# Kernel optimization log

Measured on AMD Instinct MI355X. Metric: run time of the kernel, lower is better.

Reference implementation:

```python
import jax, jax.numpy as jnp
import numpy as np

DIM = 2048
HEADS = 16
HD = DIM // HEADS  # 128
EPS = 1e-5


def layernorm(t, w, b):
    # FloatLayerNorm: LayerNorm computed in float32 over last dim
    t32 = t.astype(jnp.float32)
    mu = jnp.mean(t32, axis=-1, keepdims=True)
    var = jnp.mean(jnp.square(t32 - mu), axis=-1, keepdims=True)
    y = (t32 - mu) * jax.lax.rsqrt(var + EPS)
    return (y * w + b).astype(t.dtype)


def rope(t, f_real, f_imag):
    # t: [b, s, h, hd]; frequencies in cis form, sliced to seq length
    b, s, h, hd = t.shape
    tr = t.astype(jnp.float32).reshape(b, s, h, hd // 2, 2)
    xr, xi = tr[..., 0], tr[..., 1]
    fr = f_real[:s][None, :, None, :]  # [1, s, 1, hd/2]
    fi = f_imag[:s][None, :, None, :]
    o_r = xr * fr - xi * fi
    o_i = xr * fi + xi * fr
    return jnp.stack([o_r, o_i], axis=-1).reshape(b, s, h, hd).astype(t.dtype)


def proj_norm_rope(t, Wq, Wk, Wv, qn_w, qn_b, kn_w, kn_b, f_real, f_imag):
    b, s, _ = t.shape
    q = layernorm(t @ Wq, qn_w, qn_b).reshape(b, s, HEADS, HD)
    k = layernorm(t @ Wk, kn_w, kn_b).reshape(b, s, HEADS, HD)
    v = (t @ Wv).reshape(b, s, HEADS, HD)
    q = rope(q, f_real, f_imag)
    k = rope(k, f_real, f_imag)
    return q, k, v


def sdpa(q, k, v, scale):
    # q,k,v: [b, s, h, hd] -> out [b, s, h, hd]
    scores = jnp.einsum('bqhd,bkhd->bhqk', q, k) * scale
    probs = jax.nn.softmax(scores, axis=-1)
    return jnp.einsum('bhqk,bkhd->bqhd', probs, v)


def setup_inputs() -> dict:
    key = jax.random.key(0)
    ks = jax.random.split(key, 14)
    d = {
        'c': jax.random.normal(ks[0], (2, 256, DIM), jnp.float32),
        'x': jax.random.normal(ks[1], (2, 1792, DIM), jnp.float32),
        'f_real': jax.random.normal(ks[2], (2048, HD // 2), jnp.float32),
        'f_imag': jax.random.normal(ks[3], (2048, HD // 2), jnp.float32),
    }
    sc = 1.0 / np.sqrt(DIM)
    for i, name in enumerate(['Wq', 'Wk', 'Wv', 'Wo', 'W2q', 'W2k', 'W2v', 'W2o']):
        d[name] = jax.random.normal(ks[4 + i], (DIM, DIM), jnp.float32) * sc
    for name in ['qn_w', 'kn_w', 'q2n_w', 'k2n_w']:
        d[name] = jnp.ones((DIM,), jnp.float32)
    for name in ['qn_b', 'kn_b', 'q2n_b', 'k2n_b']:
        d[name] = jnp.zeros((DIM,), jnp.float32)
    return d


def reference(c, x, f_real, f_imag, Wq, Wk, Wv, Wo, W2q, W2k, W2v, W2o,
              qn_w, qn_b, kn_w, kn_b, q2n_w, q2n_b, k2n_w, k2n_b):
    s1 = c.shape[1]
    c_q, c_k, c_v = proj_norm_rope(c, Wq, Wk, Wv, qn_w, qn_b, kn_w, kn_b, f_real, f_imag)
    x_q, x_k, x_v = proj_norm_rope(x, W2q, W2k, W2v, q2n_w, q2n_b, k2n_w, k2n_b, f_real, f_imag)
    q = jnp.concatenate([c_q, x_q], axis=1)
    k = jnp.concatenate([c_k, x_k], axis=1)
    v = jnp.concatenate([c_v, x_v], axis=1)
    out = sdpa(q, k, v, scale=1.0 / np.sqrt(HD))  # scale_by_num_heads=True
    b, s, _, _ = out.shape
    out = out.reshape(b, s, DIM)
    c_out = out[:, :s1] @ Wo
    x_out = out[:, s1:] @ W2o
    return c_out, x_out
```

## Files before the change

kernel.cpp:

```cpp
#include <hip/hip_runtime.h>

typedef __attribute__((ext_vector_type(8))) short short8;
typedef __attribute__((ext_vector_type(4))) float f32x4;
typedef __attribute__((ext_vector_type(16))) float f32x16;

#define DEV __device__ __forceinline__

DEV unsigned short f2bf(float f) {
  unsigned int u; __builtin_memcpy(&u, &f, 4);
  u = (u + 0x7FFFu + ((u >> 16) & 1u)) >> 16;
  return (unsigned short)u;
}
DEV float bf2f(unsigned short h) {
  unsigned int u = ((unsigned int)h) << 16;
  float f; __builtin_memcpy(&f, &u, 4);
  return f;
}
DEV unsigned int cvtpk(float lo, float hi_) {
  unsigned int r;
  asm("v_cvt_pk_bf16_f32 %0, %1, %2" : "=v"(r) : "v"(lo), "v"(hi_));
  return r;
}

DEV void gload_lds16(const void* g, void* l) {
  __builtin_amdgcn_global_load_lds(
      (const __attribute__((address_space(1))) void*)g,
      (__attribute__((address_space(3))) void*)l, 16, 0, 0);
}

DEV f32x16 mfma32(short8 a, short8 b, f32x16 c) {
  return __builtin_amdgcn_mfma_f32_32x32x16_bf16(a, b, c, 0, 0, 0);
}

__global__ __launch_bounds__(256) void conv_tb(const float* __restrict__ c,
                                               const float* __restrict__ x,
                                               unsigned short* __restrict__ tb) {
  int row = blockIdx.x;
  int b = row >> 11, s = row & 2047;
  const float* src = (s < 256) ? (c + (size_t)(b * 256 + s) * 2048)
                               : (x + (size_t)(b * 1792 + (s - 256)) * 2048);
  int t = threadIdx.x;
  float4 v0 = *(const float4*)&src[t * 8];
  float4 v1 = *(const float4*)&src[t * 8 + 4];
  union { unsigned short us[8]; uint4 u; } pk;
  pk.us[0] = f2bf(v0.x); pk.us[1] = f2bf(v0.y); pk.us[2] = f2bf(v0.z); pk.us[3] = f2bf(v0.w);
  pk.us[4] = f2bf(v1.x); pk.us[5] = f2bf(v1.y); pk.us[6] = f2bf(v1.z); pk.us[7] = f2bf(v1.w);
  *(uint4*)&tb[(size_t)row * 2048 + t * 8] = pk.u;
}

__global__ __launch_bounds__(256) void trans_w(
    const float* __restrict__ w0, const float* __restrict__ w1,
    const float* __restrict__ w2, const float* __restrict__ w3,
    const float* __restrict__ w4, const float* __restrict__ w5,
    const float* __restrict__ w6, const float* __restrict__ w7,
    unsigned short* __restrict__ dstbase) {
  const float* W;
  switch (blockIdx.z) {
    case 0: W = w0; break; case 1: W = w1; break; case 2: W = w2; break; case 3: W = w3; break;
    case 4: W = w4; break; case 5: W = w5; break; case 6: W = w6; break; default: W = w7; break;
  }
  unsigned short* Wt = dstbase + (size_t)blockIdx.z * 2048 * 2048;
  __shared__ float tile[64][65];
  int n0 = blockIdx.x * 64, k0 = blockIdx.y * 64;
  int j = threadIdx.x & 63, i0 = threadIdx.x >> 6;
#pragma unroll
  for (int p = 0; p < 16; ++p) {
    int i = i0 + p * 4;
    tile[i][j] = W[(size_t)(k0 + i) * 2048 + n0 + j];
  }
  __syncthreads();
#pragma unroll
  for (int p = 0; p < 16; ++p) {
    int i = i0 + p * 4;
    Wt[(size_t)(n0 + i) * 2048 + k0 + j] = f2bf(tile[j][i]);
  }
}

__global__ __launch_bounds__(256) void gemm_qkv3(
    const unsigned short* __restrict__ A,
    const unsigned short* __restrict__ Wt,
    unsigned short* __restrict__ out) {
  __shared__ __align__(16) unsigned short As[128 * 32];
  __shared__ __align__(16) unsigned short Bs[128 * 32];
  const size_t M2 = 2048ull * 2048ull;
  const int which = blockIdx.x >> 4;
  const int m0 = blockIdx.y * 128, n0 = (blockIdx.x & 15) * 128;
  const unsigned short* Bt = Wt + (size_t)(((m0 & 2047) < 256) ? which : which + 4) * M2;
  unsigned short* C = out + (size_t)which * (4096ull * 2048ull);
  const int tid = threadIdx.x, wid = tid >> 6, lane = tid & 63;
  const int g = lane >> 4, l15 = lane & 15;
  const int wm = wid >> 1, wn = wid & 1;
  const int srow = lane >> 2, skk = (lane & 3) * 8;
  f32x4 acc[4][4] = {};
  for (int k0 = 0; k0 < 2048; k0 += 32) {
#pragma unroll
    for (int rep = 0; rep < 2; ++rep) {
      int ia = wid * 2 + rep;
      gload_lds16(&A[(size_t)(m0 + ia * 16 + srow) * 2048 + k0 + skk], (char*)As + ia * 1024);
      gload_lds16(&Bt[(size_t)(n0 + ia * 16 + srow) * 2048 + k0 + skk], (char*)Bs + ia * 1024);
    }
    __syncthreads();
    short8 a[4], bb[4];
#pragma unroll
    for (int mf = 0; mf < 4; ++mf) a[mf] = *(const short8*)&As[(wm * 64 + mf * 16 + l15) * 32 + g * 8];
#pragma unroll
    for (int nf = 0; nf < 4; ++nf) bb[nf] = *(const short8*)&Bs[(wn * 64 + nf * 16 + l15) * 32 + g * 8];
#pragma unroll
    for (int mf = 0; mf < 4; ++mf)
#pragma unroll
      for (int nf = 0; nf < 4; ++nf)
        acc[mf][nf] = __builtin_amdgcn_mfma_f32_16x16x32_bf16(a[mf], bb[nf], acc[mf][nf], 0, 0, 0);
    __syncthreads();
  }
#pragma unroll
  for (int mf = 0; mf < 4; ++mf)
#pragma unroll
    for (int r = 0; r < 4; ++r) {
      int row = m0 + wm * 64 + mf * 16 + 4 * g + r;
#pragma unroll
      for (int nf = 0; nf < 4; ++nf)
        C[(size_t)row * 2048 + n0 + wn * 64 + nf * 16 + l15] = f2bf(acc[mf][nf][r]);
    }
}

__global__ __launch_bounds__(256) void gemm_out(
    const unsigned short* __restrict__ A,
    const unsigned short* __restrict__ B1t,
    const unsigned short* __restrict__ B2t,
    float* __restrict__ Co) {
  __shared__ __align__(16) unsigned short As[128 * 32];
  __shared__ __align__(16) unsigned short Bs[128 * 32];
  const int m0 = blockIdx.y * 128, n0 = blockIdx.x * 128;
  const unsigned short* Bt = ((m0 & 2047) < 256) ? B1t : B2t;
  const int tid = threadIdx.x, wid = tid >> 6, lane = tid & 63;
  const int g = lane >> 4, l15 = lane & 15;
  const int wm = wid >> 1, wn = wid & 1;
  const int srow = lane >> 2, skk = (lane & 3) * 8;
  f32x4 acc[4][4] = {};
  for (int k0 = 0; k0 < 2048; k0 += 32) {
#pragma unroll
    for (int rep = 0; rep < 2; ++rep) {
      int ia = wid * 2 + rep;
      gload_lds16(&A[(size_t)(m0 + ia * 16 + srow) * 2048 + k0 + skk], (char*)As + ia * 1024);
      gload_lds16(&Bt[(size_t)(n0 + ia * 16 + srow) * 2048 + k0 + skk], (char*)Bs + ia * 1024);
    }
    __syncthreads();
    short8 a[4], bb[4];
#pragma unroll
    for (int mf = 0; mf < 4; ++mf) a[mf] = *(const short8*)&As[(wm * 64 + mf * 16 + l15) * 32 + g * 8];
#pragma unroll
    for (int nf = 0; nf < 4; ++nf) bb[nf] = *(const short8*)&Bs[(wn * 64 + nf * 16 + l15) * 32 + g * 8];
#pragma unroll
    for (int mf = 0; mf < 4; ++mf)
#pragma unroll
      for (int nf = 0; nf < 4; ++nf)
        acc[mf][nf] = __builtin_amdgcn_mfma_f32_16x16x32_bf16(a[mf], bb[nf], acc[mf][nf], 0, 0, 0);
    __syncthreads();
  }
#pragma unroll
  for (int mf = 0; mf < 4; ++mf)
#pragma unroll
    for (int r = 0; r < 4; ++r) {
      int row = m0 + wm * 64 + mf * 16 + 4 * g + r;
      int b = row >> 11, s = row & 2047;
      size_t dst = (s < 256) ? ((size_t)b * 256 + s) * 2048
                             : 1048576ull + ((size_t)b * 1792 + (s - 256)) * 2048;
#pragma unroll
      for (int nf = 0; nf < 4; ++nf)
        Co[dst + n0 + wn * 64 + nf * 16 + l15] = acc[mf][nf][r];
    }
}

__global__ __launch_bounds__(256) void ln_rope(
    const unsigned short* __restrict__ P,
    const float* __restrict__ w1, const float* __restrict__ b1,
    const float* __restrict__ w2, const float* __restrict__ b2,
    const float* __restrict__ fre, const float* __restrict__ fim,
    unsigned short* __restrict__ Oa, float oscale) {
  int row = blockIdx.x;
  int b = row >> 11, s = row & 2047;
  int pos = (s < 256) ? s : s - 256;
  const float* w = (s < 256) ? w1 : w2;
  const float* bb = (s < 256) ? b1 : b2;
  int t = threadIdx.x, lane = t & 63, wid = t >> 6;
  int col = t * 8;
  uint4 raw = *(const uint4*)&P[(size_t)row * 2048 + col];
  const unsigned short* rp = (const unsigned short*)&raw;
  float xv[8];
#pragma unroll
  for (int j = 0; j < 8; ++j) xv[j] = bf2f(rp[j]);
  float s1 = 0.f, s2 = 0.f;
#pragma unroll
  for (int j = 0; j < 8; ++j) { s1 += xv[j]; s2 += xv[j] * xv[j]; }
#pragma unroll
  for (int off = 32; off; off >>= 1) { s1 += __shfl_xor(s1, off); s2 += __shfl_xor(s2, off); }
  __shared__ float red1[4], red2[4];
  if (lane == 0) { red1[wid] = s1; red2[wid] = s2; }
  __syncthreads();
  s1 = red1[0] + red1[1] + red1[2] + red1[3];
  s2 = red2[0] + red2[1] + red2[2] + red2[3];
  float mean = s1 * (1.f / 2048.f);
  float var = s2 * (1.f / 2048.f) - mean * mean;
  float rs = rsqrtf(var + 1e-5f);
  float4 wv0 = *(const float4*)&w[col], wv1 = *(const float4*)&w[col + 4];
  float4 bv0 = *(const float4*)&bb[col], bv1 = *(const float4*)&bb[col + 4];
  float y[8];
  y[0] = (xv[0] - mean) * rs * wv0.x + bv0.x; y[1] = (xv[1] - mean) * rs * wv0.y + bv0.y;
  y[2] = (xv[2] - mean) * rs * wv0.z + bv0.z; y[3] = (xv[3] - mean) * rs * wv0.w + bv0.w;
  y[4] = (xv[4] - mean) * rs * wv1.x + bv1.x; y[5] = (xv[5] - mean) * rs * wv1.y + bv1.y;
  y[6] = (xv[6] - mean) * rs * wv1.z + bv1.z; y[7] = (xv[7] - mean) * rs * wv1.w + bv1.w;
#pragma unroll
  for (int j = 0; j < 8; ++j) y[j] *= oscale;
  int hd0 = col & 127;
  int i0 = hd0 >> 1;
  float4 fr = *(const float4*)&fre[(size_t)pos * 64 + i0];
  float4 fi = *(const float4*)&fim[(size_t)pos * 64 + i0];
  union { unsigned short us[8]; uint4 u; } pk;
  pk.us[0] = f2bf(y[0] * fr.x - y[1] * fi.x); pk.us[1] = f2bf(y[0] * fi.x + y[1] * fr.x);
  pk.us[2] = f2bf(y[2] * fr.y - y[3] * fi.y); pk.us[3] = f2bf(y[2] * fi.y + y[3] * fr.y);
  pk.us[4] = f2bf(y[4] * fr.z - y[5] * fi.z); pk.us[5] = f2bf(y[4] * fi.z + y[5] * fr.z);
  pk.us[6] = f2bf(y[6] * fr.w - y[7] * fi.w); pk.us[7] = f2bf(y[6] * fi.w + y[7] * fr.w);
  int h = col >> 7;
  *(uint4*)&Oa[((size_t)(b * 16 + h) * 2048 + s) * 128 + hd0] = pk.u;
}

__global__ __launch_bounds__(256) void v_trans(const unsigned short* __restrict__ vp,
                                               unsigned short* __restrict__ va) {
  int bh = blockIdx.y;
  int b = bh >> 4, h = bh & 15;
  int s0 = blockIdx.x * 64;
  __shared__ unsigned short tile[64][128];
  int tid = threadIdx.x;
#pragma unroll
  for (int p = 0; p < 4; ++p) {
    int s = p * 16 + (tid >> 4);
    int d0 = (tid & 15) * 8;
    *(uint4*)&tile[s][d0] = *(const uint4*)&vp[((size_t)b * 2048 + s0 + s) * 2048 + h * 128 + d0];
  }
  __syncthreads();
#pragma unroll
  for (int p = 0; p < 4; ++p) {
    int d = p * 32 + (tid >> 3);
    int soff = (tid & 7) * 8;
    union { unsigned short us[8]; uint4 u; } pk;
#pragma unroll
    for (int u = 0; u < 8; ++u) pk.us[u] = tile[soff + u][d];
    *(uint4*)&va[((size_t)(b * 16 + h) * 128 + d) * 2048 + s0 + soff] = pk.u;
  }
}

#define THR_LOG2 11.5f

__global__ __launch_bounds__(512) void attn_kernel(
    const unsigned short* __restrict__ Q,
    const unsigned short* __restrict__ Kb,
    const unsigned short* __restrict__ Vt,
    unsigned short* __restrict__ O) {
  __shared__ __align__(16) unsigned short smem[32768];
  const int q0 = blockIdx.x * 256;
  const int h = blockIdx.y, b = blockIdx.z;
  const int tid = threadIdx.x, wid = tid >> 6, lane = tid & 63;
  const int l31 = lane & 31, hi = lane >> 5;
  const size_t base = (size_t)(b * 16 + h) * 2048 * 128;
  const unsigned short* kbase = Kb + base;
  const unsigned short* vbase = Vt + base;

  const int qrow = q0 + wid * 32 + l31;
  short8 qf[8];
#pragma unroll
  for (int ks = 0; ks < 8; ++ks)
    qf[ks] = *(const short8*)&Q[base + (size_t)qrow * 128 + ks * 16 + hi * 8];

  f32x16 o_acc[4] = {};
  float m_run = -1e30f, l_run = 0.f;

#define STAGE(cur, kv0)                                                              \
  {                                                                                  \
_Pragma("unroll")                                                                    \
    for (int p = 0; p < 2; ++p) {                                                    \
      int slot = p * 512 + wid * 64 + lane;                                          \
      int row = slot >> 4;                                                           \
      int u = (slot & 15) ^ (row & 7);                                               \
      gload_lds16(&kbase[(size_t)((kv0) + row) * 128 + u * 8],                       \
                  (char*)(smem + (cur) * 16384) + (p * 512 + wid * 64) * 16);        \
    }                                                                                \
_Pragma("unroll")                                                                    \
    for (int p = 0; p < 2; ++p) {                                                    \
      int slot = p * 512 + wid * 64 + lane;                                          \
      int d = slot >> 3;                                                             \
      int u = (slot & 7) ^ (d & 7);                                                  \
      gload_lds16(&vbase[(size_t)d * 2048 + (kv0) + u * 8],                          \
                  (char*)(smem + (cur) * 16384 + 8192) + (p * 512 + wid * 64) * 16); \
    }                                                                                \
  }

  STAGE(0, 0)

#pragma unroll 1
  for (int t = 0; t < 32; ++t) {
    const int cur = t & 1;
    if (t < 31) {
      STAGE(cur ^ 1, (t + 1) * 64)
      asm volatile("s_waitcnt vmcnt(4)" ::: "memory");
    } else {
      asm volatile("s_waitcnt vmcnt(0)" ::: "memory");
    }
    __builtin_amdgcn_s_barrier();

    const char* Ksb = (const char*)(smem + cur * 16384);
    const char* Vsb = (const char*)(smem + cur * 16384 + 8192);

    f32x16 sT0 = {}, sT1 = {};
    __builtin_amdgcn_s_setprio(1);
#pragma unroll
    for (int ks = 0; ks < 8; ++ks) {
      int unit = ks * 2 + hi;
      int r0 = l31;
      short8 kf0 = *(const short8*)(Ksb + ((r0 * 16 + (unit ^ (r0 & 7))) << 4));
      sT0 = mfma32(kf0, qf[ks], sT0);
      int r1 = 32 + l31;
      short8 kf1 = *(const short8*)(Ksb + ((r1 * 16 + (unit ^ (r1 & 7))) << 4));
      sT1 = mfma32(kf1, qf[ks], sT1);
    }
    __builtin_amdgcn_s_setprio(0);

    float mx = sT0[0];
#pragma unroll
    for (int r = 1; r < 16; ++r) mx = fmaxf(mx, sT0[r]);
#pragma unroll
    for (int r = 0; r < 16; ++r) mx = fmaxf(mx, sT1[r]);
    mx = fmaxf(mx, __shfl_xor(mx, 32));
    if (!__all(mx <= m_run + THR_LOG2)) {
      float mn = fmaxf(m_run, mx);
      float corr = __builtin_exp2f(m_run - mn);
      m_run = mn;
      l_run *= corr;
#pragma unroll
      for (int di = 0; di < 4; ++di)
#pragma unroll
        for (int r = 0; r < 16; ++r) o_acc[di][r] *= corr;
    }
    float ts = 0.f;
#pragma unroll
    for (int r = 0; r < 16; ++r) { sT0[r] = __builtin_exp2f(sT0[r] - m_run); ts += sT0[r]; }
#pragma unroll
    for (int r = 0; r < 16; ++r) { sT1[r] = __builtin_exp2f(sT1[r] - m_run); ts += sT1[r]; }
    ts += __shfl_xor(ts, 32);
    l_run += ts;

    unsigned int w0[8], w1[8];
#pragma unroll
    for (int j = 0; j < 8; ++j) {
      w0[j] = cvtpk(sT0[2 * j], sT0[2 * j + 1]);
      w1[j] = cvtpk(sT1[2 * j], sT1[2 * j + 1]);
    }
    unsigned int y0[4], y1[4];
    y0[0] = __shfl_xor((int)(hi ? w0[0] : w0[2]), 32);
    y0[1] = __shfl_xor((int)(hi ? w0[1] : w0[3]), 32);
    y0[2] = __shfl_xor((int)(hi ? w0[4] : w0[6]), 32);
    y0[3] = __shfl_xor((int)(hi ? w0[5] : w0[7]), 32);
    y1[0] = __shfl_xor((int)(hi ? w1[0] : w1[2]), 32);
    y1[1] = __shfl_xor((int)(hi ? w1[1] : w1[3]), 32);
    y1[2] = __shfl_xor((int)(hi ? w1[4] : w1[6]), 32);
    y1[3] = __shfl_xor((int)(hi ? w1[5] : w1[7]), 32);
    union { unsigned int u[4]; short8 s8; } pf[2][2];
    pf[0][0].u[0] = hi ? y0[0] : w0[0]; pf[0][0].u[1] = hi ? y0[1] : w0[1];
    pf[0][0].u[2] = hi ? w0[2] : y0[0]; pf[0][0].u[3] = hi ? w0[3] : y0[1];
    pf[0][1].u[0] = hi ? y0[2] : w0[4]; pf[0][1].u[1] = hi ? y0[3] : w0[5];
    pf[0][1].u[2] = hi ? w0[6] : y0[2]; pf[0][1].u[3] = hi ? w0[7] : y0[3];
    pf[1][0].u[0] = hi ? y1[0] : w1[0]; pf[1][0].u[1] = hi ? y1[1] : w1[1];
    pf[1][0].u[2] = hi ? w1[2] : y1[0]; pf[1][0].u[3] = hi ? w1[3] : y1[1];
    pf[1][1].u[0] = hi ? y1[2] : w1[4]; pf[1][1].u[1] = hi ? y1[3] : w1[5];
    pf[1][1].u[2] = hi ? w1[6] : y1[2]; pf[1][1].u[3] = hi ? w1[7] : y1[3];

    __builtin_amdgcn_s_setprio(1);
#pragma unroll
    for (int di = 0; di < 4; ++di) {
      int row = di * 32 + l31;
      int sw = row & 7;
#pragma unroll
      for (int kb = 0; kb < 2; ++kb)
#pragma unroll
        for (int ks2 = 0; ks2 < 2; ++ks2) {
          int unit = kb * 4 + ks2 * 2 + hi;
          short8 vf = *(const short8*)(Vsb + ((row * 8 + (unit ^ sw)) << 4));
          o_acc[di] = mfma32(vf, pf[kb][ks2].s8, o_acc[di]);
        }
    }
    __builtin_amdgcn_s_setprio(0);
    __builtin_amdgcn_s_barrier();
  }

  float inv = 1.0f / l_run;
  char* ow = (char*)smem + wid * 8192;
#pragma unroll
  for (int di = 0; di < 4; ++di)
#pragma unroll
    for (int rg = 0; rg < 4; ++rg) {
      unsigned int lo = cvtpk(o_acc[di][rg * 4 + 0] * inv, o_acc[di][rg * 4 + 1] * inv);
      unsigned int hi_w = cvtpk(o_acc[di][rg * 4 + 2] * inv, o_acc[di][rg * 4 + 3] * inv);
      int byte = (l31 * 256 + di * 64 + rg * 16 + hi * 8) ^ ((l31 & 7) << 4);
      *(unsigned long long*)(ow + byte) =
          ((unsigned long long)hi_w << 32) | (unsigned long long)lo;
    }
  size_t obase = ((size_t)b * 2048 + q0 + wid * 32) * 2048 + (size_t)h * 128;
#pragma unroll
  for (int it = 0; it < 8; ++it) {
    int q = it * 4 + (lane >> 4);
    int d0 = (lane & 15) * 8;
    int byte = (q * 256 + d0 * 2) ^ ((q & 7) << 4);
    uint4 val = *(const uint4*)(ow + byte);
    *(uint4*)&O[obase + (size_t)q * 2048 + d0] = val;
  }
}

extern "C" void kernel_launch(void* const* d_in, const int* in_sizes, int n_in,
                              void* d_out, int out_size, void* d_ws, size_t ws_size,
                              hipStream_t stream) {
  (void)in_sizes; (void)n_in; (void)out_size; (void)ws_size;
  const float* c = (const float*)d_in[0];
  const float* x = (const float*)d_in[1];
  const float* fre = (const float*)d_in[2];
  const float* fim = (const float*)d_in[3];

  char* ws = (char*)d_ws;
  const size_t M2 = 2048ull * 2048ull;
  unsigned short* tb = (unsigned short*)ws;
  unsigned short* Wt = (unsigned short*)(ws + 16777216ull);
  unsigned short* qkv = (unsigned short*)(ws + 83886080ull);
  unsigned short* qp = qkv;
  unsigned short* kp = (unsigned short*)(ws + 100663296ull);
  unsigned short* vp = (unsigned short*)(ws + 117440512ull);
  unsigned short* qa = (unsigned short*)(ws + 134217728ull);
  unsigned short* ka = (unsigned short*)(ws + 150994944ull);
  unsigned short* va = (unsigned short*)(ws + 167772160ull);
  unsigned short* attn_out = qp;

  conv_tb<<<4096, 256, 0, stream>>>(c, x, tb);
  trans_w<<<dim3(32, 32, 8), 256, 0, stream>>>(
      (const float*)d_in[4], (const float*)d_in[5], (const float*)d_in[6], (const float*)d_in[7],
      (const float*)d_in[8], (const float*)d_in[9], (const float*)d_in[10], (const float*)d_in[11],
      Wt);
  gemm_qkv3<<<dim3(48, 32), 256, 0, stream>>>(tb, Wt, qkv);
  ln_rope<<<4096, 256, 0, stream>>>(qp, (const float*)d_in[12], (const float*)d_in[16],
                                    (const float*)d_in[14], (const float*)d_in[18], fre, fim, qa,
                                    0.08838834764831845f * 1.4426950408889634f);
  ln_rope<<<4096, 256, 0, stream>>>(kp, (const float*)d_in[13], (const float*)d_in[17],
                                    (const float*)d_in[15], (const float*)d_in[19], fre, fim, ka,
                                    1.0f);
  v_trans<<<dim3(32, 32), 256, 0, stream>>>(vp, va);
  attn_kernel<<<dim3(8, 16, 2), 512, 0, stream>>>(qa, ka, va, attn_out);
  gemm_out<<<dim3(16, 32), 256, 0, stream>>>(attn_out, Wt + 3 * M2, Wt + 7 * M2, (float*)d_out);
}
```

Measured before the change: 351.9 us.

## Rewrite QKV GEMM as 256x256-tile, 8-wave, double-buffered pipelined kernel

Replaces the 128x128, 4-wave QKV projection GEMM with a 256x256-tile, 512-thread kernel. It uses 128KB of dynamic LDS with double buffering, a K step of 64, and XOR-swizzled LDS layout to avoid bank conflicts. The K loop is split into four MFMA phases, with async global-to-LDS loads for later tiles interleaved between them and explicit waitcnt/barrier/setprio control. A block-index swizzle groups tiles for cache locality. The goal is to hide memory latency and raise MFMA utilization, in exchange for heavy LDS use (one block per CU) and fragile hand-tuned synchronization.

```diff
diff --git a/kernel.cpp b/kernel.cpp
--- a/kernel.cpp
+++ b/kernel.cpp
@@ -30,6 +30,9 @@
 
 DEV f32x16 mfma32(short8 a, short8 b, f32x16 c) {
   return __builtin_amdgcn_mfma_f32_32x32x16_bf16(a, b, c, 0, 0, 0);
+}
+DEV f32x4 mfma16(short8 a, short8 b, f32x4 c) {
+  return __builtin_amdgcn_mfma_f32_16x16x32_bf16(a, b, c, 0, 0, 0);
 }
 
 __global__ __launch_bounds__(256) void conv_tb(const float* __restrict__ c,
@@ -76,51 +79,172 @@
   }
 }
 
-__global__ __launch_bounds__(256) void gemm_qkv3(
+DEV void stage_A8(char* ldsAbase, const unsigned short* gtile, int mh, int wid, int lane) {
+#pragma unroll
+  for (int p = 0; p < 2; ++p) {
+    int row0 = mh * 64 + p * 128 + wid * 8;
+    int row = row0 + (lane >> 3);
+    int u = (lane & 7) ^ (row & 7);
+    gload_lds16(gtile + (size_t)row * 2048 + u * 8, ldsAbase + row0 * 128);
+  }
+}
+DEV void stage_B8(char* ldsBbase, const unsigned short* gtile, int nh, int wid, int lane) {
+#pragma unroll
+  for (int p = 0; p < 2; ++p) {
+    int idx = p * 8 + wid;
+    int row0 = (idx >> 2) * 64 + nh * 32 + (idx & 3) * 8;
+    int row = row0 + (lane >> 3);
+    int u = (lane & 7) ^ (row & 7);
+    gload_lds16(gtile + (size_t)row * 2048 + u * 8, ldsBbase + row0 * 128);
+  }
+}
+
+__global__ __launch_bounds__(512, 2) void gemm_qkv3_8ph(
     const unsigned short* __restrict__ A,
     const unsigned short* __restrict__ Wt,
     unsigned short* __restrict__ out) {
-  __shared__ __align__(16) unsigned short As[128 * 32];
-  __shared__ __align__(16) unsigned short Bs[128 * 32];
+  extern __shared__ __align__(16) char ldsc[];
   const size_t M2 = 2048ull * 2048ull;
-  const int which = blockIdx.x >> 4;
-  const int m0 = blockIdx.y * 128, n0 = (blockIdx.x & 15) * 128;
+  int bid = blockIdx.x;
+  int sw = (bid & 7) * 48 + (bid >> 3);
+  const int which = sw >> 7;
+  const int rem = sw & 127;
+  const int m0 = (rem >> 3) * 256, n0 = (rem & 7) * 256;
   const unsigned short* Bt = Wt + (size_t)(((m0 & 2047) < 256) ? which : which + 4) * M2;
   unsigned short* C = out + (size_t)which * (4096ull * 2048ull);
   const int tid = threadIdx.x, wid = tid >> 6, lane = tid & 63;
   const int g = lane >> 4, l15 = lane & 15;
-  const int wm = wid >> 1, wn = wid & 1;
-  const int srow = lane >> 2, skk = (lane & 3) * 8;
-  f32x4 acc[4][4] = {};
-  for (int k0 = 0; k0 < 2048; k0 += 32) {
-#pragma unroll
-    for (int rep = 0; rep < 2; ++rep) {
-      int ia = wid * 2 + rep;
-      gload_lds16(&A[(size_t)(m0 + ia * 16 + srow) * 2048 + k0 + skk], (char*)As + ia * 1024);
-      gload_lds16(&Bt[(size_t)(n0 + ia * 16 + srow) * 2048 + k0 + skk], (char*)Bs + ia * 1024);
-    }
-    __syncthreads();
-    short8 a[4], bb[4];
-#pragma unroll
-    for (int mf = 0; mf < 4; ++mf) a[mf] = *(const short8*)&As[(wm * 64 + mf * 16 + l15) * 32 + g * 8];
-#pragma unroll
-    for (int nf = 0; nf < 4; ++nf) bb[nf] = *(const short8*)&Bs[(wn * 64 + nf * 16 + l15) * 32 + g * 8];
-#pragma unroll
-    for (int mf = 0; mf < 4; ++mf)
-#pragma unroll
-      for (int nf = 0; nf < 4; ++nf)
-        acc[mf][nf] = __builtin_amdgcn_mfma_f32_16x16x32_bf16(a[mf], bb[nf], acc[mf][nf], 0, 0, 0);
-    __syncthreads();
-  }
-#pragma unroll
-  for (int mf = 0; mf < 4; ++mf)
-#pragma unroll
-    for (int r = 0; r < 4; ++r) {
-      int row = m0 + wm * 64 + mf * 16 + 4 * g + r;
-#pragma unroll
-      for (int nf = 0; nf < 4; ++nf)
-        C[(size_t)row * 2048 + n0 + wn * 64 + nf * 16 + l15] = f2bf(acc[mf][nf][r]);
-    }
+  const int wm = wid >> 2, wn = wid & 3;
+  const unsigned short* gA = A + (size_t)m0 * 2048;
+  const unsigned short* gB = Bt + (size_t)n0 * 2048;
+
+  f32x4 acc[8][4] = {};
+
+  stage_A8(ldsc, gA, 0, wid, lane);
+  stage_A8(ldsc, gA, 1, wid, lane);
+  stage_B8(ldsc + 32768, gB, 0, wid, lane);
+  stage_B8(ldsc + 32768, gB, 1, wid, lane);
+  stage_A8(ldsc + 65536, gA + 64, 0, wid, lane);
+  stage_B8(ldsc + 98304, gB + 64, 0, wid, lane);
+  asm volatile("s_waitcnt vmcnt(4)" ::: "memory");
+  __builtin_amdgcn_s_barrier();
+
+  const int NT = 32;
+#pragma unroll 1
+  for (int t = 0; t < NT; ++t) {
+    const int bufOff = (t & 1) << 16;
+    char* Ab = ldsc + bufOff;
+    char* Bb = ldsc + 32768 + bufOff;
+    char* An = ldsc + (bufOff ^ 65536);
+    char* Bn = ldsc + 32768 + (bufOff ^ 65536);
+    short8 af[4][2], bf0[2][2], bf1[2][2];
+
+#pragma unroll
+    for (int m4 = 0; m4 < 4; ++m4)
+#pragma unroll
+      for (int k2 = 0; k2 < 2; ++k2) {
+        int row = wm * 128 + m4 * 16 + l15;
+        af[m4][k2] = *(const short8*)(Ab + row * 128 + (((k2 * 4 + g) ^ (row & 7)) << 4));
+      }
+#pragma unroll
+    for (int n2 = 0; n2 < 2; ++n2)
+#pragma unroll
+      for (int k2 = 0; k2 < 2; ++k2) {
+        int row = wn * 64 + n2 * 16 + l15;
+        bf0[n2][k2] = *(const short8*)(Bb + row * 128 + (((k2 * 4 + g) ^ (row & 7)) << 4));
+      }
+    if (t + 1 < NT) stage_B8(Bn, gB + (t + 1) * 64, 1, wid, lane);
+    __builtin_amdgcn_s_barrier();
+    asm volatile("s_waitcnt lgkmcnt(0)" ::: "memory");
+    __builtin_amdgcn_sched_barrier(0);
+    __builtin_amdgcn_s_setprio(1);
+#pragma unroll
+    for (int m4 = 0; m4 < 4; ++m4)
+#pragma unroll
+      for (int n2 = 0; n2 < 2; ++n2)
+#pragma unroll
+        for (int k2 = 0; k2 < 2; ++k2)
+          acc[m4][n2] = mfma16(af[m4][k2], bf0[n2][k2], acc[m4][n2]);
+    __builtin_amdgcn_s_setprio(0);
+    __builtin_amdgcn_s_barrier();
+
+#pragma unroll
+    for (int n2 = 0; n2 < 2; ++n2)
+#pragma unroll
+      for (int k2 = 0; k2 < 2; ++k2) {
+        int row = wn * 64 + 32 + n2 * 16 + l15;
+        bf1[n2][k2] = *(const short8*)(Bb + row * 128 + (((k2 * 4 + g) ^ (row & 7)) << 4));
+      }
+    if (t + 1 < NT) stage_A8(An, gA + (t + 1) * 64, 1, wid, lane);
+    __builtin_amdgcn_s_barrier();
+    asm volatile("s_waitcnt lgkmcnt(0)" ::: "memory");
+    __builtin_amdgcn_sched_barrier(0);
+    __builtin_amdgcn_s_setprio(1);
+#pragma unroll
+    for (int m4 = 0; m4 < 4; ++m4)
+#pragma unroll
+      for (int n2 = 0; n2 < 2; ++n2)
+#pragma unroll
+        for (int k2 = 0; k2 < 2; ++k2)
+          acc[m4][2 + n2] = mfma16(af[m4][k2], bf1[n2][k2], acc[m4][2 + n2]);
+    __builtin_amdgcn_s_setprio(0);
+    __builtin_amdgcn_s_barrier();
+
+#pragma unroll
+    for (int m4 = 0; m4 < 4; ++m4)
+#pragma unroll
+      for (int k2 = 0; k2 < 2; ++k2) {
+        int row = wm * 128 + 64 + m4 * 16 + l15;
+        af[m4][k2] = *(const short8*)(Ab + row * 128 + (((k2 * 4 + g) ^ (row & 7)) << 4));
+      }
+    if (t + 2 < NT) stage_A8(Ab, gA + (t + 2) * 64, 0, wid, lane);
+    __builtin_amdgcn_s_barrier();
+    asm volatile("s_waitcnt lgkmcnt(0)" ::: "memory");
+    __builtin_amdgcn_sched_barrier(0);
+    __builtin_amdgcn_s_setprio(1);
+#pragma unroll
+    for (int m4 = 0; m4 < 4; ++m4)
+#pragma unroll
+      for (int n2 = 0; n2 < 2; ++n2)
+#pragma unroll
+        for (int k2 = 0; k2 < 2; ++k2)
+          acc[4 + m4][n2] = mfma16(af[m4][k2], bf0[n2][k2], acc[4 + m4][n2]);
+    __builtin_amdgcn_s_setprio(0);
+    __builtin_amdgcn_s_barrier();
+
+    if (t + 2 < NT) stage_B8(Bb, gB + (t + 2) * 64, 0, wid, lane);
+    __builtin_amdgcn_s_barrier();
+    __builtin_amdgcn_s_setprio(1);
+#pragma unroll
+    for (int m4 = 0; m4 < 4; ++m4)
+#pragma unroll
+      for (int n2 = 0; n2 < 2; ++n2)
+#pragma unroll
+        for (int k2 = 0; k2 < 2; ++k2)
+          acc[4 + m4][2 + n2] = mfma16(af[m4][k2], bf1[n2][k2], acc[4 + m4][2 + n2]);
+    __builtin_amdgcn_s_setprio(0);
+    if (t + 2 < NT) {
+      asm volatile("s_waitcnt vmcnt(4)" ::: "memory");
+    } else if (t + 1 < NT) {
+      asm volatile("s_waitcnt vmcnt(0)" ::: "memory");
+    }
+    __builtin_amdgcn_s_barrier();
+  }
+
+#pragma unroll
+  for (int mh = 0; mh < 2; ++mh)
+#pragma unroll
+    for (int m4 = 0; m4 < 4; ++m4)
+#pragma unroll
+      for (int r = 0; r < 4; ++r) {
+        int row = m0 + wm * 128 + mh * 64 + m4 * 16 + 4 * g + r;
+#pragma unroll
+        for (int nh = 0; nh < 2; ++nh)
+#pragma unroll
+          for (int n2 = 0; n2 < 2; ++n2)
+            C[(size_t)row * 2048 + n0 + wn * 64 + nh * 32 + n2 * 16 + l15] =
+                f2bf(acc[mh * 4 + m4][nh * 2 + n2][r]);
+      }
 }
 
 __global__ __launch_bounds__(256) void gemm_out(
@@ -436,12 +560,15 @@
   unsigned short* va = (unsigned short*)(ws + 167772160ull);
   unsigned short* attn_out = qp;
 
+  (void)hipFuncSetAttribute((const void*)gemm_qkv3_8ph,
+                            hipFuncAttributeMaxDynamicSharedMemorySize, 131072);
+
   conv_tb<<<4096, 256, 0, stream>>>(c, x, tb);
   trans_w<<<dim3(32, 32, 8), 256, 0, stream>>>(
       (const float*)d_in[4], (const float*)d_in[5], (const float*)d_in[6], (const float*)d_in[7],
       (const float*)d_in[8], (const float*)d_in[9], (const float*)d_in[10], (const float*)d_in[11],
       Wt);
-  gemm_qkv3<<<dim3(48, 32), 256, 0, stream>>>(tb, Wt, qkv);
+  gemm_qkv3_8ph<<<384, 512, 131072, stream>>>(tb, Wt, qkv);
   ln_rope<<<4096, 256, 0, stream>>>(qp, (const float*)d_in[12], (const float*)d_in[16],
                                     (const float*)d_in[14], (const float*)d_in[18], fre, fim, qa,
                                     0.08838834764831845f * 1.4426950408889634f);
```

After: 349.5 us. About the same (-0.7%).
